# Kernel tuning notes

Hardware: AMD Instinct MI355X
Metric: run time of the kernel (lower is better)

Reference implementation:

```python
import jax, jax.numpy as jnp
from jax import lax
import numpy as np

GB_MAX = 3      # BandEst guard-band upper bound
RB = 1          # refer_band
PAD = RB + 1    # refer_band + init_guard_band(1)
N_OFF = 16      # ring offsets: kernel (4,4) -> N=16
BN_EPS = 1e-5

def _ring_offsets():
    idx = np.arange(-PAD, PAD + 1)
    X, Y = np.meshgrid(idx, idx, indexing='ij')
    hp = wp = 2 * PAD + 1
    def ring(M):
        return np.concatenate([M[0:RB, 0:wp - RB].ravel(), M[0:hp - RB, wp - RB:wp].ravel(),
                               M[hp - RB:hp, RB:wp].ravel(), M[RB:hp, 0:RB].ravel()])
    return ring(X).astype(np.float32), ring(Y).astype(np.float32)

PRF_X, PRF_Y = _ring_offsets()
BLOCK = np.repeat(np.arange(4), N_OFF // 4)  # offset n -> direction block (top,right,bottom,left)


def q_shift(x, H, W, shift=1, gamma=0.25):
    B, T, C = x.shape
    img = x.transpose(0, 2, 1).reshape(B, C, H, W)
    g = int(C * gamma)
    out = jnp.zeros_like(img)
    out = out.at[:, 0:g, :, shift:].set(img[:, 0:g, :, :W - shift])
    out = out.at[:, g:2 * g, :, :W - shift].set(img[:, g:2 * g, :, shift:])
    out = out.at[:, 2 * g:3 * g, shift:, :].set(img[:, 2 * g:3 * g, :H - shift, :])
    out = out.at[:, 3 * g:4 * g, :H - shift, :].set(img[:, 3 * g:4 * g, shift:, :])
    out = out.at[:, 4 * g:].set(img[:, 4 * g:])
    return out.reshape(B, C, T).transpose(0, 2, 1)


def bi_wkv(w, u, k, v):
    # Bi-directional WKV: y_t = (sum_{i<t} e^{-(t-1-i)w + k_i} v_i + e^{u+k_t} v_t
    #                            + sum_{i>t} e^{-(i-1-t)w + k_i} v_i) / (same with v->1)
    B, T, C = k.shape
    kT = k.transpose(1, 0, 2)
    vT = v.transpose(1, 0, 2)

    def step(carry, kv):
        m, a, b = carry  # state represents e^m * (a, b): (sum exp, weighted v)
        kt, vt = kv
        out = (m, a, b)  # exclusive prefix (excludes current token)
        m2 = jnp.maximum(m - w, kt)
        e1 = jnp.exp(m - w - m2)
        e2 = jnp.exp(kt - m2)
        return (m2, e1 * a + e2, e1 * b + e2 * vt), out

    init = (jnp.full((B, C), -1e38, k.dtype), jnp.zeros((B, C), k.dtype), jnp.zeros((B, C), k.dtype))
    _, (mf, af, bf) = lax.scan(step, init, (kT, vT))
    _, (mb, ab, bb) = lax.scan(step, init, (kT[::-1], vT[::-1]))
    mb, ab, bb = mb[::-1], ab[::-1], bb[::-1]
    ms = u + kT
    M = jnp.maximum(jnp.maximum(mf, mb), ms)
    ef, eb, es = jnp.exp(mf - M), jnp.exp(mb - M), jnp.exp(ms - M)
    num = ef * bf + eb * bb + es * vT
    den = ef * af + eb * ab + es
    return (num / den).transpose(1, 0, 2)


def band_est(x, cvw, cvb, bns_v, bnb_v, chw, chb, bns_h, bnb_h):
    dn = ('NCHW', 'OIHW', 'NCHW')
    gv = lax.conv_general_dilated(x, cvw, (1, 1), ((GB_MAX, GB_MAX), (0, 0)), dimension_numbers=dn) + cvb[None, :, None, None]
    gh = lax.conv_general_dilated(x, chw, (1, 1), ((0, 0), (GB_MAX, GB_MAX)), dimension_numbers=dn) + chb[None, :, None, None]
    inv = np.float32(1.0 / np.sqrt(1.0 + BN_EPS))  # eval BN: running mean 0, var 1
    gv = gv * (bns_v * inv)[None, :, None, None] + bnb_v[None, :, None, None]
    gh = gh * (bns_h * inv)[None, :, None, None] + bnb_h[None, :, None, None]
    return jnp.concatenate([jax.nn.sigmoid(gv), jax.nn.sigmoid(gh)], 1) * (GB_MAX - 1)


def _gather(xp_flat, ix, iy, wp, h, w):
    b, c = xp_flat.shape[0], xp_flat.shape[1]
    idx = (ix * wp + iy).reshape(b, 1, -1)
    return jnp.take_along_axis(xp_flat, idx, axis=2).reshape(b, c, h, w, N_OFF)


def ada_peak(x_img, cvw, cvb, bns_v, bnb_v, chw, chb, bns_h, bnb_h):
    b, c, h, w = x_img.shape
    xp = jnp.pad(x_img, ((0, 0), (0, 0), (PAD, PAD), (PAD, PAD)), mode='edge')
    hp, wp = h + 2 * PAD, w + 2 * PAD
    xp_flat = xp.reshape(b, c, hp * wp)
    gb = band_est(x_img, cvw, cvb, bns_v, bnb_v, chw, chb, bns_h, bnb_h)  # (b,4,h,w)
    zero = jnp.zeros_like(gb[:, 0])
    mvx = jnp.stack([-gb[:, 0], zero, gb[:, 1], zero], -1)  # (b,h,w,4) per block
    mvy = jnp.stack([zero, gb[:, 3], zero, -gb[:, 2]], -1)
    move_x = mvx[..., BLOCK]  # (b,h,w,16)
    move_y = mvy[..., BLOCK]
    cx = jnp.arange(PAD, h + PAD, dtype=x_img.dtype)
    cy = jnp.arange(PAD, w + PAD, dtype=x_img.dtype)
    px = cx[None, :, None, None] + jnp.asarray(PRF_X)[None, None, None, :] + move_x
    py = cy[None, None, :, None] + jnp.asarray(PRF_Y)[None, None, None, :] + move_y
    flx = jnp.floor(lax.stop_gradient(px))
    fly = jnp.floor(lax.stop_gradient(py))
    q_lt_x = jnp.clip(flx, 0, hp - 1)
    q_lt_y = jnp.clip(fly, 0, wp - 1)
    q_rb_x = jnp.clip(flx + 1, 0, hp - 1)
    q_rb_y = jnp.clip(fly + 1, 0, wp - 1)
    pxc = jnp.clip(px, 0, hp - 1)
    pyc = jnp.clip(py, 0, wp - 1)
    g_lt = (1 + (q_lt_x - pxc)) * (1 + (q_lt_y - pyc))
    g_rb = (1 - (q_rb_x - pxc)) * (1 - (q_rb_y - pyc))
    x_lt = _gather(xp_flat, q_lt_x.astype(jnp.int32), q_lt_y.astype(jnp.int32), wp, h, w)
    x_rb = _gather(xp_flat, q_rb_x.astype(jnp.int32), q_rb_y.astype(jnp.int32), wp, h, w)
    x_r = g_lt[:, None] * x_lt + g_rb[:, None] * x_rb
    return x_img[..., None] - x_r  # (b,c,h,w,N): center-minus-reference peak feature


def setup_inputs():
    key = jax.random.key(0)
    B, H, W, C = 2, 64, 64, 192
    ks = jax.random.split(key, 16)
    s = 0.02
    return {
        'x': jax.random.normal(ks[0], (B, H * W, C), jnp.float32),
        'h': H, 'w': W,
        'mix_k': jax.random.uniform(ks[1], (1, 1, C), jnp.float32),
        'mix_v': jax.random.uniform(ks[2], (1, 1, C), jnp.float32),
        'mix_r': jax.random.uniform(ks[3], (1, 1, C), jnp.float32),
        'Wk': jax.random.normal(ks[4], (C, C), jnp.float32) * s,
        'Wv': jax.random.normal(ks[5], (C, C), jnp.float32) * s,
        'Wr': jax.random.normal(ks[6], (C, C), jnp.float32) * s,
        'Wo': jax.random.normal(ks[7], (C, C), jnp.float32) * s,
        'spatial_decay': jax.random.normal(ks[8], (C,), jnp.float32),
        'spatial_first': jax.random.normal(ks[9], (C,), jnp.float32),
        'cvw': jax.random.normal(ks[10], (2, C, 2 * GB_MAX + 1, 1), jnp.float32) * s,
        'cvb': jnp.zeros((2,), jnp.float32),
        'bns_v': jnp.ones((2,), jnp.float32),
        'bnb_v': jnp.zeros((2,), jnp.float32),
        'chw': jax.random.normal(ks[11], (2, C, 1, 2 * GB_MAX + 1), jnp.float32) * s,
        'chb': jnp.zeros((2,), jnp.float32),
        'bns_h': jnp.ones((2,), jnp.float32),
        'bnb_h': jnp.zeros((2,), jnp.float32),
    }


def reference(x, h, w, mix_k, mix_v, mix_r, Wk, Wv, Wr, Wo, spatial_decay, spatial_first,
              cvw, cvb, bns_v, bnb_v, chw, chb, bns_h, bnb_h):
    B, T, C = x.shape
    xx = q_shift(x, h, w)
    xk = x * mix_k + xx * (1 - mix_k)
    xv = x * mix_v + xx * (1 - mix_v)
    xr = x * mix_r + xx * (1 - mix_r)
    k = xk @ Wk
    v = xv @ Wv
    sr = jax.nn.sigmoid(xr @ Wr)
    # deformable peak branch (AdaPeak2D) on the token grid, pooled over the N=16 ring samples
    x_img = x.transpose(0, 2, 1).reshape(B, C, h, w)
    peak = ada_peak(x_img, cvw, cvb, bns_v, bnb_v, chw, chb, bns_h, bnb_h).mean(-1)
    v = v + peak.reshape(B, C, T).transpose(0, 2, 1)
    y = bi_wkv(spatial_decay / T, spatial_first / T, k, v)
    return (sr * y) @ Wo
```

## Files before the change

### kernel.cpp

```cpp
#include <hip/hip_runtime.h>
#include <hip/hip_bf16.h>

#define BATCH 2
#define TLEN 4096
#define CC 192
#define PADC 2
#define APAD 40
#define WPAD 265

typedef __attribute__((ext_vector_type(8))) short bf16x8;
typedef __attribute__((ext_vector_type(4))) float f32x4;

__device__ __constant__ float PRF_X[16] = {-2,-2,-2,-2, -2,-1,0,1, 2,2,2,2, -1,0,1,2};
__device__ __constant__ float PRF_Y[16] = {-2,-1,0,1, 2,2,2,2, -1,0,1,2, -2,-2,-2,-2};

__device__ __forceinline__ unsigned short f2bf(float f) {
    unsigned u = __float_as_uint(f);
    u = (u + 0x7FFF + ((u >> 16) & 1)) >> 16;
    return (unsigned short)u;
}
__device__ __forceinline__ float bf2f(unsigned short h) {
    return __uint_as_float(((unsigned)h) << 16);
}

__global__ __launch_bounds__(256) void k_wcat_t(const float* __restrict__ Wk,
                                                const float* __restrict__ Wv,
                                                const float* __restrict__ Wr,
                                                const float* __restrict__ mk,
                                                const float* __restrict__ mv,
                                                const float* __restrict__ mr,
                                                unsigned short* __restrict__ WTH,
                                                unsigned short* __restrict__ WTL) {
    int idx = blockIdx.x * 256 + threadIdx.x;
    int n = idx / 384, k = idx - n * 384;
    int sec = n / CC, nc = n - sec * CC;
    const float* W   = (sec == 0) ? Wk : (sec == 1) ? Wv : Wr;
    const float* mix = (sec == 0) ? mk : (sec == 1) ? mv : mr;
    float wv = (k < CC) ? mix[k] * W[k * CC + nc]
                        : (1.0f - mix[k - CC]) * W[(k - CC) * CC + nc];
    unsigned short h = f2bf(wv);
    WTH[idx] = h;
    WTL[idx] = f2bf(wv - bf2f(h));
}

__global__ __launch_bounds__(256) void k_prep_wo(const float* __restrict__ Wo,
                                                 unsigned short* __restrict__ WoTH,
                                                 unsigned short* __restrict__ WoTL) {
    int idx = blockIdx.x * 256 + threadIdx.x;
    int n = idx / CC, k = idx - n * CC;
    float wv = Wo[k * CC + n];
    unsigned short h = f2bf(wv);
    WoTH[idx] = h;
    WoTL[idx] = f2bf(wv - bf2f(h));
}

__global__ __launch_bounds__(256, 2) void k_gemm1_mfma(
        const float* __restrict__ x,
        const unsigned short* __restrict__ WTH, const unsigned short* __restrict__ WTL,
        float* __restrict__ ZTk, float* __restrict__ Zv, float* __restrict__ ZTr) {
    __shared__ unsigned short sAh[64 * APAD], sAl[64 * APAD];
    __shared__ unsigned short sBh[192 * APAD], sBl[192 * APAD];
    const int tid  = threadIdx.x;
    const int w    = tid >> 6;
    const int lane = tid & 63;
    const int sec  = blockIdx.x;
    const int bm   = blockIdx.y * 64;

    const int arow = tid >> 2;
    const int akc  = (tid & 3) * 8;
    const int rg   = bm + arow;
    const int t    = rg & (TLEN - 1);
    const int ri   = t >> 6, rj = t & 63;

    f32x4 acc[2][6];
#pragma unroll
    for (int i = 0; i < 2; ++i)
#pragma unroll
        for (int j = 0; j < 6; ++j) acc[i][j] = f32x4{0.f, 0.f, 0.f, 0.f};

    float4 fA0, fA1;
    uint4 rB[6];

    auto loadA = [&](int k0) {
        bool aok;
        const float* src;
        if (k0 < CC) {
            src = x + (size_t)rg * CC + k0 + akc;
            aok = true;
        } else {
            int c = k0 - CC + akc;
            int g = c / 48;
            int dr;
            if      (g == 0) { dr = -1;  aok = (rj > 0);  }
            else if (g == 1) { dr =  1;  aok = (rj < 63); }
            else if (g == 2) { dr = -64; aok = (ri > 0);  }
            else             { dr =  64; aok = (ri < 63); }
            src = x + (size_t)(rg + dr) * CC + c;
        }
        if (aok) { fA0 = *(const float4*)src; fA1 = *(const float4*)(src + 4); }
        else     { fA0 = make_float4(0.f,0.f,0.f,0.f); fA1 = fA0; }
    };
    auto loadB = [&](int k0) {
#pragma unroll
        for (int q = 0; q < 3; ++q) {
            int ch  = q * 256 + tid;
            int col = ch >> 2, kc = (ch & 3) * 8;
            size_t o = (size_t)(sec * CC + col) * 384 + k0 + kc;
            rB[q * 2]     = *(const uint4*)(WTH + o);
            rB[q * 2 + 1] = *(const uint4*)(WTL + o);
        }
    };
    auto writeS = [&]() {
        float fa[8] = {fA0.x, fA0.y, fA0.z, fA0.w, fA1.x, fA1.y, fA1.z, fA1.w};
        unsigned hu[4], lu[4];
#pragma unroll
        for (int j = 0; j < 4; ++j) {
            unsigned short h0 = f2bf(fa[2*j]),   l0 = f2bf(fa[2*j]   - bf2f(h0));
            unsigned short h1 = f2bf(fa[2*j+1]), l1 = f2bf(fa[2*j+1] - bf2f(h1));
            hu[j] = (unsigned)h0 | ((unsigned)h1 << 16);
            lu[j] = (unsigned)l0 | ((unsigned)l1 << 16);
        }
        *(uint4*)&sAh[arow * APAD + akc] = make_uint4(hu[0], hu[1], hu[2], hu[3]);
        *(uint4*)&sAl[arow * APAD + akc] = make_uint4(lu[0], lu[1], lu[2], lu[3]);
#pragma unroll
        for (int q = 0; q < 3; ++q) {
            int ch  = q * 256 + tid;
            int col = ch >> 2, kc = (ch & 3) * 8;
            *(uint4*)&sBh[col * APAD + kc] = rB[q * 2];
            *(uint4*)&sBl[col * APAD + kc] = rB[q * 2 + 1];
        }
    };

    const int wrb = (w >> 1) * 32;
    const int wcb = (w & 1) * 96;
    const int r15 = lane & 15, ksub = lane >> 4;
    const int pc8 = ksub * 8;

    loadA(0); loadB(0);
    for (int step = 0; step < 12; ++step) {
        __syncthreads();
        writeS();
        __syncthreads();
        if (step < 11) { loadA((step + 1) * 32); loadB((step + 1) * 32); }
        bf16x8 ah[2], al[2], bh[6], bl[6];
#pragma unroll
        for (int f = 0; f < 2; ++f) {
            int ra = (wrb + f * 16 + r15) * APAD + pc8;
            ah[f] = *(const bf16x8*)&sAh[ra];
            al[f] = *(const bf16x8*)&sAl[ra];
        }
#pragma unroll
        for (int f = 0; f < 6; ++f) {
            int rb = (wcb + f * 16 + r15) * APAD + pc8;
            bh[f] = *(const bf16x8*)&sBh[rb];
            bl[f] = *(const bf16x8*)&sBl[rb];
        }
#pragma unroll
        for (int fr = 0; fr < 2; ++fr)
#pragma unroll
            for (int fc = 0; fc < 6; ++fc) {
                acc[fr][fc] = __builtin_amdgcn_mfma_f32_16x16x32_bf16(ah[fr], bh[fc], acc[fr][fc], 0, 0, 0);
                acc[fr][fc] = __builtin_amdgcn_mfma_f32_16x16x32_bf16(ah[fr], bl[fc], acc[fr][fc], 0, 0, 0);
                acc[fr][fc] = __builtin_amdgcn_mfma_f32_16x16x32_bf16(al[fr], bh[fc], acc[fr][fc], 0, 0, 0);
            }
    }

    if (sec == 1) {
#pragma unroll
        for (int fr = 0; fr < 2; ++fr)
#pragma unroll
            for (int fc = 0; fc < 6; ++fc) {
                int m0  = wrb + fr * 16 + ksub * 4;
                int col = wcb + fc * 16 + r15;
                f32x4 v = acc[fr][fc];
#pragma unroll
                for (int q = 0; q < 4; ++q)
                    Zv[(size_t)(bm + m0 + q) * CC + col] = v[q];
            }
    } else {
        float* D = (sec == 0) ? ZTk : ZTr;
#pragma unroll
        for (int fr = 0; fr < 2; ++fr)
#pragma unroll
            for (int fc = 0; fc < 6; ++fc) {
                int m0  = wrb + fr * 16 + ksub * 4;
                int col = wcb + fc * 16 + r15;
                f32x4 v = acc[fr][fc];
                *(float4*)(D + (size_t)col * 8192 + bm + m0) = make_float4(v[0], v[1], v[2], v[3]);
            }
    }
}

__global__ __launch_bounds__(256, 2) void k_gemm2_mfma(
        const float* __restrict__ PT,
        const unsigned short* __restrict__ WoTH, const unsigned short* __restrict__ WoTL,
        float* __restrict__ out) {
    __shared__ unsigned short sAh[64 * APAD], sAl[64 * APAD];
    __shared__ unsigned short sBh[64 * APAD], sBl[64 * APAD];
    const int tid  = threadIdx.x;
    const int w    = tid >> 6;
    const int lane = tid & 63;
    const int bn   = blockIdx.x * 64;
    const int bm   = blockIdx.y * 64;

    const int akk = tid >> 3;
    const int am8 = (tid & 7) * 8;
    const int bcol = tid >> 2;
    const int bkc  = (tid & 3) * 8;

    f32x4 acc[2][2];
#pragma unroll
    for (int i = 0; i < 2; ++i)
#pragma unroll
        for (int j = 0; j < 2; ++j) acc[i][j] = f32x4{0.f, 0.f, 0.f, 0.f};

    float4 p0, p1;
    uint4 rbh, rbl;
    auto loadAB = [&](int k0) {
        const float* pa = PT + (size_t)(k0 + akk) * 8192 + bm + am8;
        p0 = *(const float4*)pa;
        p1 = *(const float4*)(pa + 4);
        size_t o = (size_t)(bn + bcol) * CC + k0 + bkc;
        rbh = *(const uint4*)(WoTH + o);
        rbl = *(const uint4*)(WoTL + o);
    };
    auto writeS = [&]() {
        float fa[8] = {p0.x, p0.y, p0.z, p0.w, p1.x, p1.y, p1.z, p1.w};
#pragma unroll
        for (int j = 0; j < 8; ++j) {
            unsigned short h = f2bf(fa[j]);
            sAh[(am8 + j) * APAD + akk] = h;
            sAl[(am8 + j) * APAD + akk] = f2bf(fa[j] - bf2f(h));
        }
        *(uint4*)&sBh[bcol * APAD + bkc] = rbh;
        *(uint4*)&sBl[bcol * APAD + bkc] = rbl;
    };

    const int wrb = (w >> 1) * 32;
    const int wcb = (w & 1) * 32;
    const int r15 = lane & 15, ksub = lane >> 4;
    const int pc8 = ksub * 8;

    loadAB(0);
    for (int step = 0; step < 6; ++step) {
        __syncthreads();
        writeS();
        __syncthreads();
        if (step < 5) loadAB((step + 1) * 32);
        bf16x8 ah[2], al[2], bh[2], bl[2];
#pragma unroll
        for (int f = 0; f < 2; ++f) {
            int ra = (wrb + f * 16 + r15) * APAD + pc8;
            ah[f] = *(const bf16x8*)&sAh[ra];
            al[f] = *(const bf16x8*)&sAl[ra];
            int rb = (wcb + f * 16 + r15) * APAD + pc8;
            bh[f] = *(const bf16x8*)&sBh[rb];
            bl[f] = *(const bf16x8*)&sBl[rb];
        }
#pragma unroll
        for (int fr = 0; fr < 2; ++fr)
#pragma unroll
            for (int fc = 0; fc < 2; ++fc) {
                acc[fr][fc] = __builtin_amdgcn_mfma_f32_16x16x32_bf16(ah[fr], bh[fc], acc[fr][fc], 0, 0, 0);
                acc[fr][fc] = __builtin_amdgcn_mfma_f32_16x16x32_bf16(ah[fr], bl[fc], acc[fr][fc], 0, 0, 0);
                acc[fr][fc] = __builtin_amdgcn_mfma_f32_16x16x32_bf16(al[fr], bh[fc], acc[fr][fc], 0, 0, 0);
            }
    }

#pragma unroll
    for (int fr = 0; fr < 2; ++fr)
#pragma unroll
        for (int fc = 0; fc < 2; ++fc) {
            int m0  = wrb + fr * 16 + ksub * 4;
            int col = bn + wcb + fc * 16 + r15;
            f32x4 v = acc[fr][fc];
#pragma unroll
            for (int q = 0; q < 4; ++q)
                out[(size_t)(bm + m0 + q) * CC + col] = v[q];
        }
}

__global__ __launch_bounds__(192) void k_bandpeak(const float* __restrict__ x,
                                                  const float* __restrict__ cvw,
                                                  const float* __restrict__ cvb,
                                                  const float* __restrict__ bns_v,
                                                  const float* __restrict__ bnb_v,
                                                  const float* __restrict__ chw,
                                                  const float* __restrict__ chb,
                                                  const float* __restrict__ bns_h,
                                                  const float* __restrict__ bnb_h,
                                                  float* __restrict__ Zv) {
    int pixg = blockIdx.x;
    int b   = pixg >> 12;
    int pix = pixg & 4095;
    int i = pix >> 6, j = pix & 63;
    int c = threadIdx.x;
    size_t xbase = (size_t)b * TLEN * CC;

    float sv0 = 0.f, sv1 = 0.f, sh0 = 0.f, sh1 = 0.f;
#pragma unroll
    for (int t = 0; t < 7; ++t) {
        int ii = i + t - 3;
        if (ii >= 0 && ii < 64) {
            float xv = x[xbase + (size_t)(ii * 64 + j) * CC + c];
            sv0 = fmaf(xv, cvw[(0 * CC + c) * 7 + t], sv0);
            sv1 = fmaf(xv, cvw[(1 * CC + c) * 7 + t], sv1);
        }
        int jj = j + t - 3;
        if (jj >= 0 && jj < 64) {
            float xh = x[xbase + (size_t)(i * 64 + jj) * CC + c];
            sh0 = fmaf(xh, chw[(0 * CC + c) * 7 + t], sh0);
            sh1 = fmaf(xh, chw[(1 * CC + c) * 7 + t], sh1);
        }
    }
    __shared__ float red[4][CC];
    __shared__ float gsh[4];
    red[0][c] = sv0; red[1][c] = sv1; red[2][c] = sh0; red[3][c] = sh1;
    __syncthreads();
    if (c < 64) {
#pragma unroll
        for (int r = 0; r < 4; ++r) {
            float v = red[r][c] + red[r][c + 64] + red[r][c + 128];
            v += __shfl_xor(v, 32);
            v += __shfl_xor(v, 16);
            v += __shfl_xor(v, 8);
            v += __shfl_xor(v, 4);
            v += __shfl_xor(v, 2);
            v += __shfl_xor(v, 1);
            if (c == 0) {
                const float inv = 0.9999950000374997f;
                float bias, sc, sh;
                if (r < 2) { bias = cvb[r];     sc = bns_v[r];     sh = bnb_v[r]; }
                else       { bias = chb[r - 2]; sc = bns_h[r - 2]; sh = bnb_h[r - 2]; }
                float g = (v + bias) * (sc * inv) + sh;
                gsh[r] = 2.0f / (1.0f + expf(-g));
            }
        }
    }
    __syncthreads();

    __shared__ int   l_lt[16], l_rb[16];
    __shared__ float l_glt[16], l_grb[16];
    if (c < 16) {
        int n = c, blk = n >> 2;
        float mx = (blk == 0) ? -gsh[0] : (blk == 2) ? gsh[1] : 0.0f;
        float my = (blk == 1) ?  gsh[3] : (blk == 3) ? -gsh[2] : 0.0f;
        float px = (float)(i + PADC) + PRF_X[n] + mx;
        float py = (float)(j + PADC) + PRF_Y[n] + my;
        float flx = floorf(px), fly = floorf(py);
        float qltx = fminf(fmaxf(flx, 0.f), 67.f);
        float qlty = fminf(fmaxf(fly, 0.f), 67.f);
        float qrbx = fminf(fmaxf(flx + 1.f, 0.f), 67.f);
        float qrby = fminf(fmaxf(fly + 1.f, 0.f), 67.f);
        float pxc = fminf(fmaxf(px, 0.f), 67.f);
        float pyc = fminf(fmaxf(py, 0.f), 67.f);
        float glt = (1.f + (qltx - pxc)) * (1.f + (qlty - pyc));
        float grb = (1.f - (qrbx - pxc)) * (1.f - (qrby - pyc));
        int sltx = min(max((int)qltx - PADC, 0), 63);
        int slty = min(max((int)qlty - PADC, 0), 63);
        int srbx = min(max((int)qrbx - PADC, 0), 63);
        int srby = min(max((int)qrby - PADC, 0), 63);
        l_lt[n] = sltx * 64 + slty;
        l_rb[n] = srbx * 64 + srby;
        l_glt[n] = glt;
        l_grb[n] = grb;
    }
    __syncthreads();

    float acc = 0.f;
#pragma unroll
    for (int n = 0; n < 16; ++n) {
        acc = fmaf(l_glt[n], x[xbase + (size_t)l_lt[n] * CC + c], acc);
        acc = fmaf(l_grb[n], x[xbase + (size_t)l_rb[n] * CC + c], acc);
    }
    float peak = x[xbase + (size_t)pix * CC + c] - acc * 0.0625f;
    Zv[((size_t)b * TLEN + pix) * CC + c] += peak;
}

__global__ __launch_bounds__(256) void k_transv(const float* __restrict__ Zv,
                                                float* __restrict__ ZTv) {
    __shared__ float tile[64][65];
    int tid = threadIdx.x;
    int rb = (blockIdx.x & 127) * 64;
    int cb = (blockIdx.x >> 7) * 64;
    int tr  = tid >> 4;
    int tc4 = (tid & 15) * 4;
#pragma unroll
    for (int q = 0; q < 4; ++q) {
        int r = tr + q * 16;
        float4 v = *(const float4*)(Zv + (size_t)(rb + r) * CC + cb + tc4);
        *(float4*)&tile[r][tc4] = v;
    }
    __syncthreads();
#pragma unroll
    for (int q = 0; q < 4; ++q) {
        int ccol = tr + q * 16;
        float4 o = {tile[tc4 + 0][ccol], tile[tc4 + 1][ccol],
                    tile[tc4 + 2][ccol], tile[tc4 + 3][ccol]};
        *(float4*)(ZTv + (size_t)(cb + ccol) * 8192 + rb + tc4) = o;
    }
}

__global__ __launch_bounds__(256) void k_wkv2(const float* __restrict__ ZT,
                                              float* __restrict__ PT,
                                              const float* __restrict__ sd,
                                              const float* __restrict__ sf) {
    const int NTH = 256, CH = 16;
    int c = blockIdx.x % CC;
    int b = blockIdx.x / CC;
    const float w = sd[c] * (1.0f / 4096.0f);
    const float u = sf[c] * (1.0f / 4096.0f);

    __shared__ float buf[16 * WPAD];
    __shared__ float s_m[NTH], s_a[NTH], s_b[NTH], s_L[NTH];

    int tid = threadIdx.x;
    size_t base = (size_t)c * 8192 + (size_t)b * TLEN;

    float kr[CH], vr[CH], rr[CH];

    auto coopLoad = [&](const float* src) {
#pragma unroll
        for (int i = 0; i < 4; ++i) {
            int g = i * 1024 + tid * 4;
            float4 v = *(const float4*)(src + g);
            int jj0 = g & 15;
            int tp  = g >> 4;
            buf[(jj0 + 0) * WPAD + tp] = v.x;
            buf[(jj0 + 1) * WPAD + tp] = v.y;
            buf[(jj0 + 2) * WPAD + tp] = v.z;
            buf[(jj0 + 3) * WPAD + tp] = v.w;
        }
    };
    auto chunkRead = [&](float* dst) {
#pragma unroll
        for (int jj = 0; jj < CH; ++jj) dst[jj] = buf[jj * WPAD + tid];
    };

    coopLoad(ZT + base);                                __syncthreads();
    chunkRead(kr);                                      __syncthreads();
    coopLoad(ZT + (size_t)CC * 8192 + base);            __syncthreads();
    chunkRead(vr);                                      __syncthreads();
    coopLoad(ZT + (size_t)2 * CC * 8192 + base);        __syncthreads();
    chunkRead(rr);                                      __syncthreads();

    float m = -1e38f, a = 0.f, bb = 0.f;
#pragma unroll
    for (int jj = 0; jj < CH; ++jj) {
        float kt = kr[jj], vt = vr[jj];
        float m2 = fmaxf(m - w, kt);
        float e1 = expf(m - w - m2);
        float e2 = expf(kt - m2);
        a = e1 * a + e2;
        bb = e1 * bb + e2 * vt;
        m = m2;
    }
    s_m[tid] = m; s_a[tid] = a; s_b[tid] = bb; s_L[tid] = (float)CH;
    float L = (float)CH;
    for (int d = 1; d < NTH; d <<= 1) {
        __syncthreads();
        float pm = 0, pa = 0, pb = 0, pL = 0;
        bool has = (tid >= d);
        if (has) { pm = s_m[tid - d]; pa = s_a[tid - d]; pb = s_b[tid - d]; pL = s_L[tid - d]; }
        __syncthreads();
        if (has) {
            float pdec = pm - L * w;
            float m2 = fmaxf(pdec, m);
            float e1 = expf(pdec - m2);
            float e2 = expf(m - m2);
            a  = e1 * pa + e2 * a;
            bb = e1 * pb + e2 * bb;
            m = m2; L += pL;
            s_m[tid] = m; s_a[tid] = a; s_b[tid] = bb; s_L[tid] = L;
        }
    }
    __syncthreads();
    float fm = -1e38f, fa = 0.f, fb = 0.f;
    if (tid > 0) { fm = s_m[tid - 1]; fa = s_a[tid - 1]; fb = s_b[tid - 1]; }
    __syncthreads();

    m = -1e38f; a = 0.f; bb = 0.f;
#pragma unroll
    for (int jj = CH - 1; jj >= 0; --jj) {
        float kt = kr[jj], vt = vr[jj];
        float m2 = fmaxf(m - w, kt);
        float e1 = expf(m - w - m2);
        float e2 = expf(kt - m2);
        a = e1 * a + e2;
        bb = e1 * bb + e2 * vt;
        m = m2;
    }
    s_m[tid] = m; s_a[tid] = a; s_b[tid] = bb; s_L[tid] = (float)CH;
    L = (float)CH;
    for (int d = 1; d < NTH; d <<= 1) {
        __syncthreads();
        float pm = 0, pa = 0, pb = 0, pL = 0;
        bool has = (tid + d) < NTH;
        if (has) { pm = s_m[tid + d]; pa = s_a[tid + d]; pb = s_b[tid + d]; pL = s_L[tid + d]; }
        __syncthreads();
        if (has) {
            float pdec = pm - L * w;
            float m2 = fmaxf(m, pdec);
            float e1 = expf(m - m2);
            float e2 = expf(pdec - m2);
            a  = e1 * a + e2 * pa;
            bb = e1 * bb + e2 * pb;
            m = m2; L += pL;
            s_m[tid] = m; s_a[tid] = a; s_b[tid] = bb; s_L[tid] = L;
        }
    }
    __syncthreads();
    float bm2 = -1e38f, ba = 0.f, bbv = 0.f;
    if (tid < NTH - 1) { bm2 = s_m[tid + 1]; ba = s_a[tid + 1]; bbv = s_b[tid + 1]; }
    __syncthreads();

    float em[CH], ea[CH], eb[CH];
    m = bm2; a = ba; bb = bbv;
#pragma unroll
    for (int jj = CH - 1; jj >= 0; --jj) {
        em[jj] = m; ea[jj] = a; eb[jj] = bb;
        float kt = kr[jj], vt = vr[jj];
        float m2 = fmaxf(m - w, kt);
        float e1 = expf(m - w - m2);
        float e2 = expf(kt - m2);
        a = e1 * a + e2;
        bb = e1 * bb + e2 * vt;
        m = m2;
    }

    m = fm; a = fa; bb = fb;
#pragma unroll
    for (int jj = 0; jj < CH; ++jj) {
        float kt = kr[jj], vt = vr[jj];
        float ms = u + kt;
        float M = fmaxf(fmaxf(m, em[jj]), ms);
        float ef  = expf(m - M);
        float ebk = expf(em[jj] - M);
        float es  = expf(ms - M);
        float num = ef * bb + ebk * eb[jj] + es * vt;
        float den = ef * a + ebk * ea[jj] + es;
        float y = num / den;
        float sr = 1.0f / (1.0f + expf(-rr[jj]));
        buf[jj * WPAD + tid] = sr * y;
        float m2 = fmaxf(m - w, kt);
        float e1 = expf(m - w - m2);
        float e2 = expf(kt - m2);
        a = e1 * a + e2;
        bb = e1 * bb + e2 * vt;
        m = m2;
    }
    __syncthreads();
#pragma unroll
    for (int i = 0; i < 4; ++i) {
        int g = i * 1024 + tid * 4;
        int jj0 = g & 15;
        int tp  = g >> 4;
        float4 o = {buf[(jj0 + 0) * WPAD + tp], buf[(jj0 + 1) * WPAD + tp],
                    buf[(jj0 + 2) * WPAD + tp], buf[(jj0 + 3) * WPAD + tp]};
        *(float4*)(PT + base + g) = o;
    }
}

extern "C" void kernel_launch(void* const* d_in, const int* in_sizes, int n_in,
                              void* d_out, int out_size, void* d_ws, size_t ws_size,
                              hipStream_t stream) {
    const float* x     = (const float*)d_in[0];
    const float* mix_k = (const float*)d_in[3];
    const float* mix_v = (const float*)d_in[4];
    const float* mix_r = (const float*)d_in[5];
    const float* Wk    = (const float*)d_in[6];
    const float* Wv    = (const float*)d_in[7];
    const float* Wr    = (const float*)d_in[8];
    const float* Wo    = (const float*)d_in[9];
    const float* sd    = (const float*)d_in[10];
    const float* sf    = (const float*)d_in[11];
    const float* cvw   = (const float*)d_in[12];
    const float* cvb   = (const float*)d_in[13];
    const float* bns_v = (const float*)d_in[14];
    const float* bnb_v = (const float*)d_in[15];
    const float* chw   = (const float*)d_in[16];
    const float* chb   = (const float*)d_in[17];
    const float* bns_h = (const float*)d_in[18];
    const float* bnb_h = (const float*)d_in[19];
    float* out = (float*)d_out;
    char* W = (char*)d_ws;

    float*          Zv   = (float*)(W + 0);
    float*          ZTk  = (float*)(W + 6291456);
    float*          ZTv  = (float*)(W + 12582912);
    float*          ZTr  = (float*)(W + 18874368);
    float*          PT   = Zv;
    unsigned short* WTH  = (unsigned short*)(W + 25165824);
    unsigned short* WTL  = (unsigned short*)(W + 25608192);
    unsigned short* WoTH = (unsigned short*)(W + 26050560);
    unsigned short* WoTL = (unsigned short*)(W + 26124288);

    k_wcat_t<<<864, 256, 0, stream>>>(Wk, Wv, Wr, mix_k, mix_v, mix_r, WTH, WTL);
    k_prep_wo<<<144, 256, 0, stream>>>(Wo, WoTH, WoTL);
    k_gemm1_mfma<<<dim3(3, 128), 256, 0, stream>>>(x, WTH, WTL, ZTk, Zv, ZTr);
    k_bandpeak<<<8192, 192, 0, stream>>>(x, cvw, cvb, bns_v, bnb_v, chw, chb, bns_h, bnb_h, Zv);
    k_transv<<<384, 256, 0, stream>>>(Zv, ZTv);
    k_wkv2<<<384, 256, 0, stream>>>(ZTk, PT, sd, sf);
    k_gemm2_mfma<<<dim3(3, 128), 256, 0, stream>>>(PT, WoTH, WoTL, out);
}
```

Measured before the change: 234.1 us.

## Double-buffer LDS in first GEMM and split output columns across two blocks

Measured after the change: 223.9 us. 4.3% less time.

```diff
diff --git a/kernel.cpp b/kernel.cpp
--- a/kernel.cpp
+++ b/kernel.cpp
@@ -58,13 +58,15 @@
         const float* __restrict__ x,
         const unsigned short* __restrict__ WTH, const unsigned short* __restrict__ WTL,
         float* __restrict__ ZTk, float* __restrict__ Zv, float* __restrict__ ZTr) {
-    __shared__ unsigned short sAh[64 * APAD], sAl[64 * APAD];
-    __shared__ unsigned short sBh[192 * APAD], sBl[192 * APAD];
+    __shared__ unsigned short sAh[2][64 * APAD], sAl[2][64 * APAD];
+    __shared__ unsigned short sBh[2][96 * APAD], sBl[2][96 * APAD];
     const int tid  = threadIdx.x;
     const int w    = tid >> 6;
     const int lane = tid & 63;
-    const int sec  = blockIdx.x;
+    const int sec  = blockIdx.x >> 1;
+    const int half = blockIdx.x & 1;
     const int bm   = blockIdx.y * 64;
+    const int gcb  = sec * CC + half * 96;
 
     const int arow = tid >> 2;
     const int akc  = (tid & 3) * 8;
@@ -72,14 +74,14 @@
     const int t    = rg & (TLEN - 1);
     const int ri   = t >> 6, rj = t & 63;
 
-    f32x4 acc[2][6];
+    f32x4 acc[2][3];
 #pragma unroll
     for (int i = 0; i < 2; ++i)
 #pragma unroll
-        for (int j = 0; j < 6; ++j) acc[i][j] = f32x4{0.f, 0.f, 0.f, 0.f};
+        for (int j = 0; j < 3; ++j) acc[i][j] = f32x4{0.f, 0.f, 0.f, 0.f};
 
     float4 fA0, fA1;
-    uint4 rB[6];
+    uint4 rB[4];
 
     auto loadA = [&](int k0) {
         bool aok;
@@ -101,16 +103,21 @@
         else     { fA0 = make_float4(0.f,0.f,0.f,0.f); fA1 = fA0; }
     };
     auto loadB = [&](int k0) {
-#pragma unroll
-        for (int q = 0; q < 3; ++q) {
-            int ch  = q * 256 + tid;
+        {
+            int col = tid >> 2, kc = (tid & 3) * 8;
+            size_t o = (size_t)(gcb + col) * 384 + k0 + kc;
+            rB[0] = *(const uint4*)(WTH + o);
+            rB[1] = *(const uint4*)(WTL + o);
+        }
+        if (tid < 128) {
+            int ch = 256 + tid;
             int col = ch >> 2, kc = (ch & 3) * 8;
-            size_t o = (size_t)(sec * CC + col) * 384 + k0 + kc;
-            rB[q * 2]     = *(const uint4*)(WTH + o);
-            rB[q * 2 + 1] = *(const uint4*)(WTL + o);
+            size_t o = (size_t)(gcb + col) * 384 + k0 + kc;
+            rB[2] = *(const uint4*)(WTH + o);
+            rB[3] = *(const uint4*)(WTL + o);
         }
     };
-    auto writeS = [&]() {
+    auto writeS = [&](int buf) {
         float fa[8] = {fA0.x, fA0.y, fA0.z, fA0.w, fA1.x, fA1.y, fA1.z, fA1.w};
         unsigned hu[4], lu[4];
 #pragma unroll
@@ -120,58 +127,68 @@
             hu[j] = (unsigned)h0 | ((unsigned)h1 << 16);
             lu[j] = (unsigned)l0 | ((unsigned)l1 << 16);
         }
-        *(uint4*)&sAh[arow * APAD + akc] = make_uint4(hu[0], hu[1], hu[2], hu[3]);
-        *(uint4*)&sAl[arow * APAD + akc] = make_uint4(lu[0], lu[1], lu[2], lu[3]);
-#pragma unroll
-        for (int q = 0; q < 3; ++q) {
-            int ch  = q * 256 + tid;
+        *(uint4*)&sAh[buf][arow * APAD + akc] = make_uint4(hu[0], hu[1], hu[2], hu[3]);
+        *(uint4*)&sAl[buf][arow * APAD + akc] = make_uint4(lu[0], lu[1], lu[2], lu[3]);
+        {
+            int col = tid >> 2, kc = (tid & 3) * 8;
+            *(uint4*)&sBh[buf][col * APAD + kc] = rB[0];
+            *(uint4*)&sBl[buf][col * APAD + kc] = rB[1];
+        }
+        if (tid < 128) {
+            int ch = 256 + tid;
             int col = ch >> 2, kc = (ch & 3) * 8;
-            *(uint4*)&sBh[col * APAD + kc] = rB[q * 2];
-            *(uint4*)&sBl[col * APAD + kc] = rB[q * 2 + 1];
+            *(uint4*)&sBh[buf][col * APAD + kc] = rB[2];
+            *(uint4*)&sBl[buf][col * APAD + kc] = rB[3];
         }
     };
 
     const int wrb = (w >> 1) * 32;
-    const int wcb = (w & 1) * 96;
+    const int wcb = (w & 1) * 48;
     const int r15 = lane & 15, ksub = lane >> 4;
     const int pc8 = ksub * 8;
 
     loadA(0); loadB(0);
+    writeS(0);
+    __syncthreads();
+
+    int buf = 0;
     for (int step = 0; step < 12; ++step) {
-        __syncthreads();
-        writeS();
-        __syncthreads();
         if (step < 11) { loadA((step + 1) * 32); loadB((step + 1) * 32); }
-        bf16x8 ah[2], al[2], bh[6], bl[6];
+        bf16x8 ah[2], al[2], bh[3], bl[3];
 #pragma unroll
         for (int f = 0; f < 2; ++f) {
             int ra = (wrb + f * 16 + r15) * APAD + pc8;
-            ah[f] = *(const bf16x8*)&sAh[ra];
-            al[f] = *(const bf16x8*)&sAl[ra];
-        }
-#pragma unroll
-        for (int f = 0; f < 6; ++f) {
+            ah[f] = *(const bf16x8*)&sAh[buf][ra];
+            al[f] = *(const bf16x8*)&sAl[buf][ra];
+        }
+#pragma unroll
+        for (int f = 0; f < 3; ++f) {
             int rb = (wcb + f * 16 + r15) * APAD + pc8;
-            bh[f] = *(const bf16x8*)&sBh[rb];
-            bl[f] = *(const bf16x8*)&sBl[rb];
+            bh[f] = *(const bf16x8*)&sBh[buf][rb];
+            bl[f] = *(const bf16x8*)&sBl[buf][rb];
         }
 #pragma unroll
         for (int fr = 0; fr < 2; ++fr)
 #pragma unroll
-            for (int fc = 0; fc < 6; ++fc) {
+            for (int fc = 0; fc < 3; ++fc) {
                 acc[fr][fc] = __builtin_amdgcn_mfma_f32_16x16x32_bf16(ah[fr], bh[fc], acc[fr][fc], 0, 0, 0);
                 acc[fr][fc] = __builtin_amdgcn_mfma_f32_16x16x32_bf16(ah[fr], bl[fc], acc[fr][fc], 0, 0, 0);
                 acc[fr][fc] = __builtin_amdgcn_mfma_f32_16x16x32_bf16(al[fr], bh[fc], acc[fr][fc], 0, 0, 0);
             }
+        if (step < 11) {
+            writeS(buf ^ 1);
+            __syncthreads();
+            buf ^= 1;
+        }
     }
 
     if (sec == 1) {
 #pragma unroll
         for (int fr = 0; fr < 2; ++fr)
 #pragma unroll
-            for (int fc = 0; fc < 6; ++fc) {
+            for (int fc = 0; fc < 3; ++fc) {
                 int m0  = wrb + fr * 16 + ksub * 4;
-                int col = wcb + fc * 16 + r15;
+                int col = half * 96 + wcb + fc * 16 + r15;
                 f32x4 v = acc[fr][fc];
 #pragma unroll
                 for (int q = 0; q < 4; ++q)
@@ -182,9 +199,9 @@
 #pragma unroll
         for (int fr = 0; fr < 2; ++fr)
 #pragma unroll
-            for (int fc = 0; fc < 6; ++fc) {
+            for (int fc = 0; fc < 3; ++fc) {
                 int m0  = wrb + fr * 16 + ksub * 4;
-                int col = wcb + fc * 16 + r15;
+                int col = half * 96 + wcb + fc * 16 + r15;
                 f32x4 v = acc[fr][fc];
                 *(float4*)(D + (size_t)col * 8192 + bm + m0) = make_float4(v[0], v[1], v[2], v[3]);
             }
@@ -597,7 +614,7 @@
 
     k_wcat_t<<<864, 256, 0, stream>>>(Wk, Wv, Wr, mix_k, mix_v, mix_r, WTH, WTL);
     k_prep_wo<<<144, 256, 0, stream>>>(Wo, WoTH, WoTL);
-    k_gemm1_mfma<<<dim3(3, 128), 256, 0, stream>>>(x, WTH, WTL, ZTk, Zv, ZTr);
+    k_gemm1_mfma<<<dim3(6, 128), 256, 0, stream>>>(x, WTH, WTL, ZTk, Zv, ZTr);
     k_bandpeak<<<8192, 192, 0, stream>>>(x, cvw, cvb, bns_v, bnb_v, chw, chb, bns_h, bnb_h, Zv);
     k_transv<<<384, 256, 0, stream>>>(Zv, ZTv);
     k_wkv2<<<384, 256, 0, stream>>>(ZTk, PT, sd, sf);
```
